# Optimization experiments

Hardware: AMD Instinct MI355X
Metric: run time of the kernel (lower is better)

## Reference

```python
import jax, jax.numpy as jnp
import numpy as np

N = 50000        # nodes
E = 600000       # edges (before self-loops)
IN_DIM = 128
HID = 128
EMB = 128
DEC = 64
B = 1024         # drug pairs
NEG_GAT = 0.2    # GATConv leaky-relu slope
NEG_DEC = 0.1    # decoder LeakyReLU slope
EPS = 1e-5       # BatchNorm eps


def setup_inputs() -> dict:
    key = jax.random.key(0)
    ks = jax.random.split(key, 16)
    rn = lambda k, s, sc=0.05: jax.random.normal(k, s, dtype=jnp.float32) * sc
    return dict(
        x=rn(ks[0], (N, IN_DIM), 1.0),
        edge_index=jax.random.randint(ks[1], (2, E), 0, N, dtype=jnp.int32),
        drug_index=jax.random.randint(ks[2], (B, 2), 1, N + 1, dtype=jnp.int32),
        W1=rn(ks[3], (HID, IN_DIM)), att1=rn(ks[4], (1, 1, 2 * HID)), b1=jnp.zeros((HID,), jnp.float32),
        g1=jnp.ones((HID,), jnp.float32), be1=jnp.zeros((HID,), jnp.float32),
        W2=rn(ks[5], (HID, HID)), att2=rn(ks[6], (1, 1, 2 * HID)), b2=jnp.zeros((HID,), jnp.float32),
        g2=jnp.ones((HID,), jnp.float32), be2=jnp.zeros((HID,), jnp.float32),
        W3=rn(ks[7], (EMB, HID)), att3=rn(ks[8], (1, 1, 2 * EMB)), b3=jnp.zeros((EMB,), jnp.float32),
        g3=jnp.ones((EMB,), jnp.float32), be3=jnp.zeros((EMB,), jnp.float32),
        P1=rn(ks[9], (EMB, DEC), 0.1), P2=rn(ks[10], (DEC, DEC), 0.1),
    )


def _segment_softmax(alpha, seg, n):
    amax = jax.ops.segment_max(alpha, seg, num_segments=n)
    amax = jnp.where(jnp.isfinite(amax), amax, 0.0)
    ex = jnp.exp(alpha - amax[seg])
    den = jax.ops.segment_sum(ex, seg, num_segments=n)
    return ex / (den[seg] + 1e-16)


def _gat(x, src, dst, W, att, b):
    # num_head == 1 (required by original att-parameter shape)
    n = x.shape[0]
    d = W.shape[0]
    h = (x @ W.T)[:, None, :]                    # [N,1,d]
    x_i, x_j = h[dst], h[src]                    # target, source per edge
    # alpha = (cat([x_i,x_j],-1)*att).sum(-1) without materializing the concat
    alpha = (x_i * att[..., :d]).sum(-1) + (x_j * att[..., d:]).sum(-1)  # [E,1]
    alpha = jax.nn.leaky_relu(alpha, NEG_GAT)
    # NOTE: original code softmaxes over edge_index[0] (src) while aggregating by dst
    alpha = _segment_softmax(alpha, src, n)
    out = jax.ops.segment_sum(x_j * alpha[:, :, None], dst, num_segments=n)
    return jax.nn.relu(out.reshape(n, -1) + b)


def _bn(x, g, b):
    # BatchNorm1d (training-mode batch statistics, biased var)
    mu = x.mean(0)
    var = x.var(0)
    return (x - mu) * jax.lax.rsqrt(var + EPS) * g + b


def reference(x, edge_index, drug_index, W1, att1, b1, g1, be1,
              W2, att2, b2, g2, be2, W3, att3, b3, g3, be3, P1, P2):
    n = x.shape[0]
    loops = jnp.arange(n, dtype=edge_index.dtype)
    src = jnp.concatenate([edge_index[0], loops])  # add_self_loops
    dst = jnp.concatenate([edge_index[1], loops])
    h = jax.nn.leaky_relu(_bn(_gat(x, src, dst, W1, att1, b1), g1, be1), NEG_DEC)
    h = jax.nn.leaky_relu(_bn(_gat(h, src, dst, W2, att2, b2), g2, be2), NEG_DEC)
    h = jax.nn.leaky_relu(_bn(_gat(h, src, dst, W3, att3, b3), g3, be3), NEG_DEC)
    a = h[drug_index[:, 0] - 1]                    # [B,EMB]
    bvec = h[drug_index[:, 1] - 1]                 # [B,EMB]
    M = P1 @ P2 @ P1.T                             # [EMB,EMB] bilinear form
    ypred = jnp.einsum('bd,de,be->b', a, M, bvec)[:, None]  # [B,1]
    return ypred
```

## Files before the change

### kernel.cpp

```cpp
#include <hip/hip_runtime.h>
#include <hip/hip_bf16.h>

#define DEVINL __device__ __forceinline__

constexpr int N  = 50000;
constexpr int E  = 600000;
constexpr int TE = E + N;
constexpr int D  = 128;
constexpr int SCAN_B = (N + 255) / 256;
constexpr int GEMM_ROWS = 64;
constexpr int GEMM_B = (N + GEMM_ROWS - 1) / GEMM_ROWS;
constexpr int HST_STRIDE = 136;

typedef short bf16x8 __attribute__((ext_vector_type(8)));
typedef float f32x4  __attribute__((ext_vector_type(4)));

DEVINL float lrelu(float x, float s) { return x >= 0.f ? x : s * x; }

DEVINL unsigned short f2bf(float f) {
    unsigned u = __float_as_uint(f);
    u += 0x7FFFu + ((u >> 16) & 1u);
    return (unsigned short)(u >> 16);
}
DEVINL float bfl(unsigned u) { return __uint_as_float(u << 16); }
DEVINL float bfh(unsigned u) { return __uint_as_float(u & 0xFFFF0000u); }

__global__ __launch_bounds__(256) void k_wb3(const float* __restrict__ W0,
                                             const float* __restrict__ W1,
                                             const float* __restrict__ W2,
                                             unsigned short* __restrict__ Wb) {
    int b = blockIdx.x;
    int l = b >> 6;
    const float* W = (l == 0) ? W0 : (l == 1) ? W1 : W2;
    int t = (b & 63) * 256 + threadIdx.x;
    Wb[l * 16384 + t] = f2bf(W[t]);
}

__global__ __launch_bounds__(256) void k_gemm(const float* __restrict__ X,
                                              const unsigned short* __restrict__ O16,
                                              const unsigned short* __restrict__ Wb,
                                              unsigned short* __restrict__ Hb16,
                                              const float* __restrict__ att,
                                              float* __restrict__ ai,
                                              float* __restrict__ ajx,
                                              const float* __restrict__ csum,
                                              const float* __restrict__ csq,
                                              const float* __restrict__ g,
                                              const float* __restrict__ be,
                                              int apply_bn) {
    __shared__ unsigned short hst[4][16][HST_STRIDE];
    __shared__ float ssl[256];
    int wave = threadIdx.x >> 6, lane = threadIdx.x & 63;
    int m = lane & 15, quad = lane >> 4;
    int r0 = blockIdx.x * GEMM_ROWS + wave * 16;

    if (apply_bn) {
        if (threadIdx.x < 128) {
            int c = threadIdx.x;
            float mean = csum[c] / (float)N;
            float var  = csq[c] / (float)N - mean * mean;
            float scale = g[c] * rsqrtf(var + 1e-5f);
            ssl[c] = scale;
            ssl[128 + c] = be[c] - mean * scale;
        }
        __syncthreads();
    }

    bf16x8 afrag[4];
    int rowA = r0 + m;
    bool rowok = rowA < N;
    #pragma unroll
    for (int k4 = 0; k4 < 4; k4++) {
        int c0 = k4 * 32 + quad * 8;
        float v[8];
        if (rowok) {
            if (apply_bn) {
                uint4 hu = *(const uint4*)(O16 + (size_t)rowA * D + c0);
                v[0] = bfl(hu.x); v[1] = bfh(hu.x);
                v[2] = bfl(hu.y); v[3] = bfh(hu.y);
                v[4] = bfl(hu.z); v[5] = bfh(hu.z);
                v[6] = bfl(hu.w); v[7] = bfh(hu.w);
                #pragma unroll
                for (int j = 0; j < 8; j++)
                    v[j] = lrelu(v[j] * ssl[c0 + j] + ssl[128 + c0 + j], 0.1f);
            } else {
                float4 x0 = *(const float4*)(X + (size_t)rowA * D + c0);
                float4 x1 = *(const float4*)(X + (size_t)rowA * D + c0 + 4);
                v[0] = x0.x; v[1] = x0.y; v[2] = x0.z; v[3] = x0.w;
                v[4] = x1.x; v[5] = x1.y; v[6] = x1.z; v[7] = x1.w;
            }
        } else {
            #pragma unroll
            for (int j = 0; j < 8; j++) v[j] = 0.f;
        }
        #pragma unroll
        for (int j = 0; j < 8; j++) afrag[k4][j] = (short)f2bf(v[j]);
    }

    float pii[4] = {0.f, 0.f, 0.f, 0.f};
    float pjj[4] = {0.f, 0.f, 0.f, 0.f};
    #pragma unroll
    for (int nt = 0; nt < 8; nt++) {
        int n0 = nt * 16;
        f32x4 acc = {0.f, 0.f, 0.f, 0.f};
        const unsigned short* wrow = Wb + (size_t)(n0 + m) * D + quad * 8;
        #pragma unroll
        for (int k4 = 0; k4 < 4; k4++) {
            bf16x8 b = *(const bf16x8*)(wrow + k4 * 32);
            acc = __builtin_amdgcn_mfma_f32_16x16x32_bf16(afrag[k4], b, acc, 0, 0, 0);
        }
        float ad = att[n0 + m];
        float as = att[128 + n0 + m];
        #pragma unroll
        for (int i = 0; i < 4; i++) {
            hst[wave][quad * 4 + i][n0 + m] = f2bf(acc[i]);
            pii[i] += acc[i] * ad;
            pjj[i] += acc[i] * as;
        }
    }

    #pragma unroll
    for (int t = 0; t < 4; t++) {
        int r = t * 4 + quad;
        int row = r0 + r;
        int cb = m * 8;
        uint4 vv = *(const uint4*)&hst[wave][r][cb];
        if (row < N)
            *(uint4*)(Hb16 + (size_t)row * D + cb) = vv;
    }

    #pragma unroll
    for (int mask = 8; mask >= 1; mask >>= 1) {
        #pragma unroll
        for (int i = 0; i < 4; i++) {
            pii[i] += __shfl_xor(pii[i], mask);
            pjj[i] += __shfl_xor(pjj[i], mask);
        }
    }
    if (m == 0) {
        #pragma unroll
        for (int i = 0; i < 4; i++) {
            int row = r0 + quad * 4 + i;
            if (row < N) { ai[row] = pii[i]; ajx[2 * (size_t)row] = pjj[i]; }
        }
    }
}

DEVINL void edge_sd(int e, const int* ei, int& s, int& d) {
    if (e < E) { s = ei[e]; d = ei[E + e]; }
    else       { s = d = e - E; }
}

__global__ __launch_bounds__(256) void k_deg2(const int* __restrict__ ei,
                                              int* __restrict__ degd,
                                              int* __restrict__ degs,
                                              unsigned* __restrict__ rpack) {
    int e = blockIdx.x * 256 + threadIdx.x;
    if (e >= TE) return;
    int s, d; edge_sd(e, ei, s, d);
    int rd = atomicAdd(degd + d, 1);
    int rs = atomicAdd(degs + s, 1);
    rpack[e] = (unsigned)(rd & 0xFFFF) | ((unsigned)rs << 16);
}

__global__ __launch_bounds__(256) void k_scan1(const int* __restrict__ degbase, int* __restrict__ bsum) {
    __shared__ int red[256];
    int arr = blockIdx.x >= SCAN_B;
    int b   = blockIdx.x - arr * SCAN_B;
    const int* deg = degbase + (size_t)arr * N;
    int t = threadIdx.x;
    int v = b * 256 + t;
    red[t] = (v < N) ? deg[v] : 0;
    __syncthreads();
    #pragma unroll
    for (int off = 128; off; off >>= 1) {
        if (t < off) red[t] += red[t + off];
        __syncthreads();
    }
    if (t == 0) bsum[arr * 256 + b] = red[0];
}

__global__ __launch_bounds__(256) void k_scan2(const int* __restrict__ bsum,
                                               int* __restrict__ boff, int* __restrict__ ptrbase) {
    __shared__ int sc[256];
    int t = threadIdx.x;
    for (int arr = 0; arr < 2; arr++) {
        int v = (t < SCAN_B) ? bsum[arr * 256 + t] : 0;
        sc[t] = v;
        __syncthreads();
        #pragma unroll
        for (int off = 1; off < 256; off <<= 1) {
            int add = (t >= off) ? sc[t - off] : 0;
            __syncthreads();
            sc[t] += add;
            __syncthreads();
        }
        if (t < SCAN_B) boff[arr * 256 + t] = sc[t] - v;
        if (t == SCAN_B - 1) ptrbase[(size_t)arr * (N + 8) + N] = sc[t];
        __syncthreads();
    }
}

__global__ __launch_bounds__(256) void k_scan3(const int* __restrict__ degbase,
                                               const int* __restrict__ boff,
                                               int* __restrict__ ptrbase) {
    __shared__ int sc[256];
    int arr = blockIdx.x >= SCAN_B;
    int b   = blockIdx.x - arr * SCAN_B;
    const int* deg = degbase + (size_t)arr * N;
    int* ptr       = ptrbase + (size_t)arr * (N + 8);
    int t = threadIdx.x;
    int v = b * 256 + t;
    int d = (v < N) ? deg[v] : 0;
    sc[t] = d;
    __syncthreads();
    #pragma unroll
    for (int off = 1; off < 256; off <<= 1) {
        int add = (t >= off) ? sc[t - off] : 0;
        __syncthreads();
        sc[t] += add;
        __syncthreads();
    }
    if (v < N) ptr[v] = boff[arr * 256 + b] + sc[t] - d;
}

__global__ __launch_bounds__(256) void k_fill2(const int* __restrict__ ei,
                                               const int* __restrict__ rowp,
                                               const int* __restrict__ srcp,
                                               const unsigned* __restrict__ rpack,
                                               unsigned short* __restrict__ srcc,
                                               unsigned short* __restrict__ dstc) {
    int e = blockIdx.x * 256 + threadIdx.x;
    if (e >= TE) return;
    int s, d; edge_sd(e, ei, s, d);
    unsigned rp = rpack[e];
    srcc[rowp[d] + (int)(rp & 0xFFFFu)] = (unsigned short)s;
    dstc[srcp[s] + (int)(rp >> 16)]     = (unsigned short)d;
}

__global__ __launch_bounds__(256) void k_den(const int* __restrict__ srcp,
                                             const unsigned short* __restrict__ dstc,
                                             const float* __restrict__ ai,
                                             float* __restrict__ ajx,
                                             float* __restrict__ csumz) {
    if (blockIdx.x == 0) csumz[threadIdx.x] = 0.f;
    int g = threadIdx.x >> 4, l16 = threadIdx.x & 15;
    int v = blockIdx.x * 16 + g;
    if (v >= N) return;
    int beg = srcp[v], end = srcp[v + 1];
    float ajv = ajx[2 * (size_t)v];
    float acc = 0.f;
    for (int idx = beg + l16; idx < end; idx += 16) {
        int d = dstc[idx];
        acc += expf(lrelu(ai[d] + ajv, 0.2f));
    }
    #pragma unroll
    for (int mask = 8; mask >= 1; mask >>= 1) acc += __shfl_xor(acc, mask);
    if (l16 == 0) ajx[2 * (size_t)v + 1] = 1.0f / (acc + 1e-16f);
}

__global__ __launch_bounds__(256) void k_aggregate(const int* __restrict__ rowp,
                                                   const unsigned short* __restrict__ srcc,
                                                   const float* __restrict__ ai,
                                                   const float2* __restrict__ ajinv,
                                                   const uint2* __restrict__ Hu2,
                                                   const float* __restrict__ bvec,
                                                   unsigned short* __restrict__ O16) {
    int wid = threadIdx.x >> 6, lane = threadIdx.x & 63;
    int h = lane >> 5, l32 = lane & 31;
    int v = blockIdx.x * 4 + wid;
    if (v >= N) return;
    int beg = rowp[v], end = rowp[v + 1];
    float aiv = ai[v];
    float a0 = 0.f, a1 = 0.f, a2 = 0.f, a3 = 0.f;
    int idx = beg;
    for (; idx + 8 <= end; idx += 8) {
        int    s[4];
        float2 aw[4];
        uint2  u[4];
        #pragma unroll
        for (int t = 0; t < 4; t++) s[t] = srcc[idx + 2 * t + h];
        #pragma unroll
        for (int t = 0; t < 4; t++) aw[t] = ajinv[s[t]];
        #pragma unroll
        for (int t = 0; t < 4; t++) u[t] = Hu2[(size_t)s[t] * 32 + l32];
        #pragma unroll
        for (int t = 0; t < 4; t++) {
            float w = expf(lrelu(aiv + aw[t].x, 0.2f)) * aw[t].y;
            a0 += w * bfl(u[t].x);
            a1 += w * bfh(u[t].x);
            a2 += w * bfl(u[t].y);
            a3 += w * bfh(u[t].y);
        }
    }
    for (; idx + 2 <= end; idx += 2) {
        int s = srcc[idx + h];
        float2 aw = ajinv[s];
        float w = expf(lrelu(aiv + aw.x, 0.2f)) * aw.y;
        uint2 u = Hu2[(size_t)s * 32 + l32];
        a0 += w * bfl(u.x);
        a1 += w * bfh(u.x);
        a2 += w * bfl(u.y);
        a3 += w * bfh(u.y);
    }
    if (idx < end) {
        int s = srcc[idx];
        float2 aw = ajinv[s];
        float w = (h == 0) ? expf(lrelu(aiv + aw.x, 0.2f)) * aw.y : 0.f;
        uint2 u = Hu2[(size_t)s * 32 + l32];
        a0 += w * bfl(u.x);
        a1 += w * bfh(u.x);
        a2 += w * bfl(u.y);
        a3 += w * bfh(u.y);
    }
    a0 += __shfl_xor(a0, 32);
    a1 += __shfl_xor(a1, 32);
    a2 += __shfl_xor(a2, 32);
    a3 += __shfl_xor(a3, 32);
    if (h == 0) {
        float4 b = ((const float4*)bvec)[l32];
        float o0 = fmaxf(a0 + b.x, 0.f);
        float o1 = fmaxf(a1 + b.y, 0.f);
        float o2 = fmaxf(a2 + b.z, 0.f);
        float o3 = fmaxf(a3 + b.w, 0.f);
        uint2 st;
        st.x = (unsigned)f2bf(o0) | ((unsigned)f2bf(o1) << 16);
        st.y = (unsigned)f2bf(o2) | ((unsigned)f2bf(o3) << 16);
        *(uint2*)(O16 + (size_t)v * D + l32 * 4) = st;
    }
}

__global__ __launch_bounds__(256) void k_stats(const unsigned short* __restrict__ O16,
                                               float* __restrict__ colsum, float* __restrict__ colsq) {
    int c4 = (threadIdx.x & 31) * 4;
    int rg = threadIdx.x >> 5;
    float s0=0.f,s1=0.f,s2=0.f,s3=0.f,q0=0.f,q1=0.f,q2=0.f,q3=0.f;
    for (int v = blockIdx.x * 8 + rg; v < N; v += gridDim.x * 8) {
        uint2 u = *(const uint2*)(O16 + (size_t)v * D + c4);
        float v0 = bfl(u.x), v1 = bfh(u.x), v2 = bfl(u.y), v3 = bfh(u.y);
        s0 += v0; q0 += v0 * v0;
        s1 += v1; q1 += v1 * v1;
        s2 += v2; q2 += v2 * v2;
        s3 += v3; q3 += v3 * v3;
    }
    __shared__ float ls[8][128], lq[8][128];
    ls[rg][c4+0]=s0; ls[rg][c4+1]=s1; ls[rg][c4+2]=s2; ls[rg][c4+3]=s3;
    lq[rg][c4+0]=q0; lq[rg][c4+1]=q1; lq[rg][c4+2]=q2; lq[rg][c4+3]=q3;
    __syncthreads();
    if (threadIdx.x < 128) {
        int c = threadIdx.x;
        float s = 0.f, q = 0.f;
        #pragma unroll
        for (int r = 0; r < 8; r++) { s += ls[r][c]; q += lq[r][c]; }
        atomicAdd(colsum + c, s);
        atomicAdd(colsq + c, q);
    }
}

__global__ __launch_bounds__(256) void k_T(const float* __restrict__ P1, const float* __restrict__ P2,
                                           float* __restrict__ T) {
    int t = blockIdx.x * 256 + threadIdx.x;
    if (t >= 128 * 64) return;
    int i = t >> 6, d = t & 63;
    float s = 0.f;
    #pragma unroll 8
    for (int k = 0; k < 64; k++) s += P1[i * 64 + k] * P2[k * 64 + d];
    T[t] = s;
}

__global__ __launch_bounds__(256) void k_M(const float* __restrict__ T, const float* __restrict__ P1,
                                           float* __restrict__ M) {
    int t = blockIdx.x * 256 + threadIdx.x;
    if (t >= 128 * 128) return;
    int i = t >> 7, j = t & 127;
    float s = 0.f;
    #pragma unroll 8
    for (int d = 0; d < 64; d++) s += T[i * 64 + d] * P1[j * 64 + d];
    M[t] = s;
}

__global__ __launch_bounds__(128) void k_pred(const unsigned short* __restrict__ O16,
                                              const float* __restrict__ csum,
                                              const float* __restrict__ csq,
                                              const float* __restrict__ g,
                                              const float* __restrict__ be,
                                              const int* __restrict__ drug,
                                              const float* __restrict__ M,
                                              float* __restrict__ out) {
    int b = blockIdx.x, i = threadIdx.x;
    __shared__ float av[128], bv[128];
    int ia = drug[b * 2] - 1, ib = drug[b * 2 + 1] - 1;
    float mean = csum[i] / (float)N;
    float var  = csq[i] / (float)N - mean * mean;
    float scale = g[i] * rsqrtf(var + 1e-5f);
    float shift = be[i] - mean * scale;
    float ha = __uint_as_float(((unsigned)O16[(size_t)ia * D + i]) << 16);
    float hb = __uint_as_float(((unsigned)O16[(size_t)ib * D + i]) << 16);
    av[i] = lrelu(ha * scale + shift, 0.1f);
    bv[i] = lrelu(hb * scale + shift, 0.1f);
    __syncthreads();
    const float4* M4  = (const float4*)(M + (size_t)i * 128);
    const float4* bv4 = (const float4*)bv;
    float u = 0.f;
    #pragma unroll 8
    for (int j = 0; j < 32; j++) {
        float4 mv = M4[j];
        float4 bb = bv4[j];
        u += mv.x * bb.x + mv.y * bb.y + mv.z * bb.z + mv.w * bb.w;
    }
    float val = av[i] * u;
    #pragma unroll
    for (int off = 32; off; off >>= 1) val += __shfl_down(val, off);
    __shared__ float red[2];
    if ((i & 63) == 0) red[i >> 6] = val;
    __syncthreads();
    if (i == 0) out[b] = red[0] + red[1];
}

extern "C" void kernel_launch(void* const* d_in, const int* in_sizes, int n_in,
                              void* d_out, int out_size, void* d_ws, size_t ws_size,
                              hipStream_t stream) {
    const float* x    = (const float*)d_in[0];
    const int*   ei   = (const int*)  d_in[1];
    const int*   drug = (const int*)  d_in[2];
    const float* W[3]   = {(const float*)d_in[3], (const float*)d_in[8],  (const float*)d_in[13]};
    const float* att[3] = {(const float*)d_in[4], (const float*)d_in[9],  (const float*)d_in[14]};
    const float* bb[3]  = {(const float*)d_in[5], (const float*)d_in[10], (const float*)d_in[15]};
    const float* gg[3]  = {(const float*)d_in[6], (const float*)d_in[11], (const float*)d_in[16]};
    const float* be[3]  = {(const float*)d_in[7], (const float*)d_in[12], (const float*)d_in[17]};
    const float* P1 = (const float*)d_in[18];
    const float* P2 = (const float*)d_in[19];

    float* ws = (float*)d_ws;
    size_t o_H      = 0;
    size_t o_O      = o_H + (size_t)N * 64;
    size_t o_ai     = o_O + (size_t)N * 64;
    size_t o_ajinv  = o_ai + N;
    size_t o_colsum = o_ajinv + 2 * (size_t)N;
    size_t o_colsq  = o_colsum + 128;
    size_t o_deg    = o_colsq + 128;
    size_t o_rpack  = o_deg + 2 * (size_t)N;
    size_t o_rowptr = o_rpack + TE;
    size_t o_srcp   = o_rowptr + N + 8;
    size_t o_src    = o_srcp + N + 8;
    size_t o_dstc   = o_src + TE / 2 + 8;
    size_t o_bsum   = o_dstc + TE / 2 + 8;
    size_t o_boff   = o_bsum + 512;
    size_t o_T      = o_boff + 512;
    size_t o_Mm     = o_T + 128 * 64;
    size_t o_Wb     = o_Mm + 128 * 128;

    unsigned short* Hb16 = (unsigned short*)(ws + o_H);
    uint2*          Hu2  = (uint2*)(ws + o_H);
    unsigned short* O16  = (unsigned short*)(ws + o_O);
    float*    ai    = ws + o_ai;
    float*    ajx   = ws + o_ajinv;
    float2*   ajinv = (float2*)(ws + o_ajinv);
    float*    csum  = ws + o_colsum;
    float*    csq   = ws + o_colsq;
    int*      degd  = (int*)(ws + o_deg);
    int*      degs  = degd + N;
    unsigned* rpack = (unsigned*)(ws + o_rpack);
    int*      rowp  = (int*)(ws + o_rowptr);
    int*      srcp  = (int*)(ws + o_srcp);
    unsigned short* srcc = (unsigned short*)(ws + o_src);
    unsigned short* dstc = (unsigned short*)(ws + o_dstc);
    int*      bsum  = (int*)(ws + o_bsum);
    int*      boff  = (int*)(ws + o_boff);
    float*    Tm    = ws + o_T;
    float*    Mm    = ws + o_Mm;
    unsigned short* Wb = (unsigned short*)(ws + o_Wb);

    const int EB = (TE + 255) / 256;
    const int NB4  = (N + 3) / 4;
    const int NB16 = (N + 15) / 16;

    hipMemsetAsync(degd, 0, (size_t)2 * N * 4, stream);
    k_deg2<<<EB, 256, 0, stream>>>(ei, degd, degs, rpack);
    k_scan1<<<2 * SCAN_B, 256, 0, stream>>>(degd, bsum);
    k_scan2<<<1, 256, 0, stream>>>(bsum, boff, rowp);
    k_scan3<<<2 * SCAN_B, 256, 0, stream>>>(degd, boff, rowp);
    k_fill2<<<EB, 256, 0, stream>>>(ei, rowp, srcp, rpack, srcc, dstc);

    k_wb3<<<192, 256, 0, stream>>>(W[0], W[1], W[2], Wb);

    for (int l = 0; l < 3; l++) {
        k_gemm<<<GEMM_B, 256, 0, stream>>>(x, O16, Wb + l * 16384, Hb16, att[l],
                                           ai, ajx, csum, csq, gg[l == 0 ? 0 : l - 1],
                                           be[l == 0 ? 0 : l - 1], l > 0 ? 1 : 0);
        k_den<<<NB16, 256, 0, stream>>>(srcp, dstc, ai, ajx, csum);
        k_aggregate<<<NB4, 256, 0, stream>>>(rowp, srcc, ai, ajinv, Hu2, bb[l], O16);
        k_stats<<<256, 256, 0, stream>>>(O16, csum, csq);
    }

    k_T<<<32, 256, 0, stream>>>(P1, P2, Tm);
    k_M<<<64, 256, 0, stream>>>(Tm, P1, Mm);
    k_pred<<<1024, 128, 0, stream>>>(O16, csum, csq, gg[2], be[2], drug, Mm, (float*)d_out);
}
```

Measured before the change: 434.1 us.

## Partition degree-count atomics per XCD with workgroup-scope atomics

```diff
diff --git a/kernel.cpp b/kernel.cpp
--- a/kernel.cpp
+++ b/kernel.cpp
@@ -7,6 +7,7 @@
 constexpr int E  = 600000;
 constexpr int TE = E + N;
 constexpr int D  = 128;
+constexpr int NXCD = 8;
 constexpr int SCAN_B = (N + 255) / 256;
 constexpr int GEMM_ROWS = 64;
 constexpr int GEMM_B = (N + GEMM_ROWS - 1) / GEMM_ROWS;
@@ -152,25 +153,41 @@
 }
 
 __global__ __launch_bounds__(256) void k_deg2(const int* __restrict__ ei,
-                                              int* __restrict__ degd,
-                                              int* __restrict__ degs,
+                                              int* __restrict__ part,
                                               unsigned* __restrict__ rpack) {
     int e = blockIdx.x * 256 + threadIdx.x;
     if (e >= TE) return;
+    unsigned xcd;
+    asm volatile("s_getreg_b32 %0, hwreg(HW_REG_XCC_ID)" : "=s"(xcd));
+    xcd &= (NXCD - 1);
     int s, d; edge_sd(e, ei, s, d);
-    int rd = atomicAdd(degd + d, 1);
-    int rs = atomicAdd(degs + s, 1);
-    rpack[e] = (unsigned)(rd & 0xFFFF) | ((unsigned)rs << 16);
-}
-
-__global__ __launch_bounds__(256) void k_scan1(const int* __restrict__ degbase, int* __restrict__ bsum) {
+    int rd = __hip_atomic_fetch_add(part + ((size_t)xcd * N + d), 1,
+                                    __ATOMIC_RELAXED, __HIP_MEMORY_SCOPE_WORKGROUP);
+    int rs = __hip_atomic_fetch_add(part + (((size_t)NXCD + xcd) * N + s), 1,
+                                    __ATOMIC_RELAXED, __HIP_MEMORY_SCOPE_WORKGROUP);
+    rpack[e] = (unsigned)rd | ((unsigned)rs << 13) | (xcd << 26);
+}
+
+__global__ __launch_bounds__(256) void k_scan1(const int* __restrict__ part,
+                                               int* __restrict__ deg,
+                                               unsigned short* __restrict__ cumx,
+                                               int* __restrict__ bsum) {
     __shared__ int red[256];
     int arr = blockIdx.x >= SCAN_B;
     int b   = blockIdx.x - arr * SCAN_B;
-    const int* deg = degbase + (size_t)arr * N;
     int t = threadIdx.x;
     int v = b * 256 + t;
-    red[t] = (v < N) ? deg[v] : 0;
+    int run = 0;
+    if (v < N) {
+        #pragma unroll
+        for (int x = 0; x < NXCD; x++) {
+            size_t o = ((size_t)arr * NXCD + x) * N + v;
+            cumx[o] = (unsigned short)run;
+            run += part[o];
+        }
+        deg[(size_t)arr * N + v] = run;
+    }
+    red[t] = run;
     __syncthreads();
     #pragma unroll
     for (int off = 128; off; off >>= 1) {
@@ -228,14 +245,20 @@
                                                const int* __restrict__ rowp,
                                                const int* __restrict__ srcp,
                                                const unsigned* __restrict__ rpack,
+                                               const unsigned short* __restrict__ cumx,
                                                unsigned short* __restrict__ srcc,
                                                unsigned short* __restrict__ dstc) {
     int e = blockIdx.x * 256 + threadIdx.x;
     if (e >= TE) return;
     int s, d; edge_sd(e, ei, s, d);
     unsigned rp = rpack[e];
-    srcc[rowp[d] + (int)(rp & 0xFFFFu)] = (unsigned short)s;
-    dstc[srcp[s] + (int)(rp >> 16)]     = (unsigned short)d;
+    int rd  = (int)(rp & 0x1FFFu);
+    int rs  = (int)((rp >> 13) & 0x1FFFu);
+    int xcd = (int)(rp >> 26);
+    int posd = rowp[d] + (int)cumx[(size_t)xcd * N + d] + rd;
+    int poss = srcp[s] + (int)cumx[((size_t)NXCD + xcd) * N + s] + rs;
+    srcc[posd] = (unsigned short)s;
+    dstc[poss] = (unsigned short)d;
 }
 
 __global__ __launch_bounds__(256) void k_den(const int* __restrict__ srcp,
@@ -438,8 +461,10 @@
     size_t o_ajinv  = o_ai + N;
     size_t o_colsum = o_ajinv + 2 * (size_t)N;
     size_t o_colsq  = o_colsum + 128;
-    size_t o_deg    = o_colsq + 128;
-    size_t o_rpack  = o_deg + 2 * (size_t)N;
+    size_t o_part   = o_colsq + 128;
+    size_t o_deg    = o_part + 2 * NXCD * (size_t)N;
+    size_t o_cumx   = o_deg + 2 * (size_t)N;
+    size_t o_rpack  = o_cumx + NXCD * (size_t)N;
     size_t o_rowptr = o_rpack + TE;
     size_t o_srcp   = o_rowptr + N + 8;
     size_t o_src    = o_srcp + N + 8;
@@ -458,8 +483,9 @@
     float2*   ajinv = (float2*)(ws + o_ajinv);
     float*    csum  = ws + o_colsum;
     float*    csq   = ws + o_colsq;
-    int*      degd  = (int*)(ws + o_deg);
-    int*      degs  = degd + N;
+    int*      part  = (int*)(ws + o_part);
+    int*      deg   = (int*)(ws + o_deg);
+    unsigned short* cumx = (unsigned short*)(ws + o_cumx);
     unsigned* rpack = (unsigned*)(ws + o_rpack);
     int*      rowp  = (int*)(ws + o_rowptr);
     int*      srcp  = (int*)(ws + o_srcp);
@@ -475,12 +501,12 @@
     const int NB4  = (N + 3) / 4;
     const int NB16 = (N + 15) / 16;
 
-    hipMemsetAsync(degd, 0, (size_t)2 * N * 4, stream);
-    k_deg2<<<EB, 256, 0, stream>>>(ei, degd, degs, rpack);
-    k_scan1<<<2 * SCAN_B, 256, 0, stream>>>(degd, bsum);
+    hipMemsetAsync(part, 0, (size_t)2 * NXCD * N * 4, stream);
+    k_deg2<<<EB, 256, 0, stream>>>(ei, part, rpack);
+    k_scan1<<<2 * SCAN_B, 256, 0, stream>>>(part, deg, cumx, bsum);
     k_scan2<<<1, 256, 0, stream>>>(bsum, boff, rowp);
-    k_scan3<<<2 * SCAN_B, 256, 0, stream>>>(degd, boff, rowp);
-    k_fill2<<<EB, 256, 0, stream>>>(ei, rowp, srcp, rpack, srcc, dstc);
+    k_scan3<<<2 * SCAN_B, 256, 0, stream>>>(deg, boff, rowp);
+    k_fill2<<<EB, 256, 0, stream>>>(ei, rowp, srcp, rpack, cumx, srcc, dstc);
 
     k_wb3<<<192, 256, 0, stream>>>(W[0], W[1], W[2], Wb);
 
```

New measurement: 432.4 us. No clear change (-0.4%).

## Build CSR via two-level bucket sort with shared-memory atomics

Applied to the files above, without the earlier changes.

```diff
diff --git a/kernel.cpp b/kernel.cpp
--- a/kernel.cpp
+++ b/kernel.cpp
@@ -7,10 +7,15 @@
 constexpr int E  = 600000;
 constexpr int TE = E + N;
 constexpr int D  = 128;
-constexpr int SCAN_B = (N + 255) / 256;
 constexpr int GEMM_ROWS = 64;
 constexpr int GEMM_B = (N + GEMM_ROWS - 1) / GEMM_ROWS;
 constexpr int HST_STRIDE = 136;
+
+constexpr int NBUCK = (N + 255) >> 8;
+constexpr int NSB   = 2 * NBUCK;
+constexpr int CHUNK = 2560;
+constexpr int EB3   = (TE + CHUNK - 1) / CHUNK;
+constexpr int EB3P  = 256;
 
 typedef short bf16x8 __attribute__((ext_vector_type(8)));
 typedef float f32x4  __attribute__((ext_vector_type(4)));
@@ -151,91 +156,133 @@
     else       { s = d = e - E; }
 }
 
-__global__ __launch_bounds__(256) void k_deg2(const int* __restrict__ ei,
-                                              int* __restrict__ degd,
-                                              int* __restrict__ degs,
-                                              unsigned* __restrict__ rpack) {
-    int e = blockIdx.x * 256 + threadIdx.x;
-    if (e >= TE) return;
-    int s, d; edge_sd(e, ei, s, d);
-    int rd = atomicAdd(degd + d, 1);
-    int rs = atomicAdd(degs + s, 1);
-    rpack[e] = (unsigned)(rd & 0xFFFF) | ((unsigned)rs << 16);
-}
-
-__global__ __launch_bounds__(256) void k_scan1(const int* __restrict__ degbase, int* __restrict__ bsum) {
-    __shared__ int red[256];
-    int arr = blockIdx.x >= SCAN_B;
-    int b   = blockIdx.x - arr * SCAN_B;
-    const int* deg = degbase + (size_t)arr * N;
+__global__ __launch_bounds__(256) void k_cnt(const int* __restrict__ ei,
+                                             unsigned* __restrict__ hist) {
+    __shared__ unsigned cnt[NSB];
+    for (int t = threadIdx.x; t < NSB; t += 256) cnt[t] = 0;
+    __syncthreads();
+    int base = blockIdx.x * CHUNK;
+    for (int i = threadIdx.x; i < CHUNK; i += 256) {
+        int e = base + i;
+        if (e < TE) {
+            int s, d; edge_sd(e, ei, s, d);
+            atomicAdd(&cnt[d >> 8], 1u);
+            atomicAdd(&cnt[NBUCK + (s >> 8)], 1u);
+        }
+    }
+    __syncthreads();
+    unsigned* row = hist + (size_t)blockIdx.x * NSB;
+    for (int t = threadIdx.x; t < NSB; t += 256) row[t] = cnt[t];
+}
+
+__global__ __launch_bounds__(256) void k_bscan(const unsigned* __restrict__ hist,
+                                               unsigned* __restrict__ pref,
+                                               unsigned* __restrict__ btot) {
+    __shared__ unsigned sc[256];
+    int sb = blockIdx.x, t = threadIdx.x;
+    unsigned v = (t < EB3) ? hist[(size_t)t * NSB + sb] : 0;
+    sc[t] = v;
+    __syncthreads();
+    #pragma unroll
+    for (int off = 1; off < 256; off <<= 1) {
+        unsigned add = (t >= off) ? sc[t - off] : 0;
+        __syncthreads();
+        sc[t] += add;
+        __syncthreads();
+    }
+    if (t < EB3) pref[(size_t)sb * EB3P + t] = sc[t] - v;
+    if (t == EB3 - 1) btot[sb] = sc[t];
+}
+
+__global__ __launch_bounds__(256) void k_boff(const unsigned* __restrict__ btot,
+                                              unsigned* __restrict__ boff2,
+                                              int* __restrict__ ptrbase) {
+    __shared__ unsigned sc[256];
     int t = threadIdx.x;
-    int v = b * 256 + t;
-    red[t] = (v < N) ? deg[v] : 0;
-    __syncthreads();
-    #pragma unroll
-    for (int off = 128; off; off >>= 1) {
-        if (t < off) red[t] += red[t + off];
-        __syncthreads();
-    }
-    if (t == 0) bsum[arr * 256 + b] = red[0];
-}
-
-__global__ __launch_bounds__(256) void k_scan2(const int* __restrict__ bsum,
-                                               int* __restrict__ boff, int* __restrict__ ptrbase) {
-    __shared__ int sc[256];
-    int t = threadIdx.x;
-    for (int arr = 0; arr < 2; arr++) {
-        int v = (t < SCAN_B) ? bsum[arr * 256 + t] : 0;
+    for (int side = 0; side < 2; side++) {
+        unsigned v = (t < NBUCK) ? btot[side * NBUCK + t] : 0;
         sc[t] = v;
         __syncthreads();
         #pragma unroll
         for (int off = 1; off < 256; off <<= 1) {
-            int add = (t >= off) ? sc[t - off] : 0;
+            unsigned add = (t >= off) ? sc[t - off] : 0;
             __syncthreads();
             sc[t] += add;
             __syncthreads();
         }
-        if (t < SCAN_B) boff[arr * 256 + t] = sc[t] - v;
-        if (t == SCAN_B - 1) ptrbase[(size_t)arr * (N + 8) + N] = sc[t];
-        __syncthreads();
-    }
-}
-
-__global__ __launch_bounds__(256) void k_scan3(const int* __restrict__ degbase,
-                                               const int* __restrict__ boff,
-                                               int* __restrict__ ptrbase) {
-    __shared__ int sc[256];
-    int arr = blockIdx.x >= SCAN_B;
-    int b   = blockIdx.x - arr * SCAN_B;
-    const int* deg = degbase + (size_t)arr * N;
-    int* ptr       = ptrbase + (size_t)arr * (N + 8);
-    int t = threadIdx.x;
-    int v = b * 256 + t;
-    int d = (v < N) ? deg[v] : 0;
-    sc[t] = d;
+        if (t < NBUCK) boff2[side * (NBUCK + 1) + t] = sc[t] - v;
+        if (t == NBUCK - 1) boff2[side * (NBUCK + 1) + NBUCK] = sc[t];
+        __syncthreads();
+    }
+    if (t == 0) { ptrbase[N] = TE; ptrbase[(N + 8) + N] = TE; }
+}
+
+__global__ __launch_bounds__(256) void k_scatter(const int* __restrict__ ei,
+                                                 const unsigned* __restrict__ pref,
+                                                 const unsigned* __restrict__ boff2,
+                                                 unsigned* __restrict__ sorted) {
+    __shared__ unsigned alloc[NSB];
+    int j = blockIdx.x;
+    for (int t = threadIdx.x; t < NSB; t += 256) {
+        int side = t >= NBUCK;
+        int bucket = t - side * NBUCK;
+        alloc[t] = boff2[side * (NBUCK + 1) + bucket] + pref[(size_t)t * EB3P + j]
+                 + (side ? (unsigned)TE : 0u);
+    }
+    __syncthreads();
+    int base = j * CHUNK;
+    for (int i = threadIdx.x; i < CHUNK; i += 256) {
+        int e = base + i;
+        if (e < TE) {
+            int s, d; edge_sd(e, ei, s, d);
+            unsigned pd = atomicAdd(&alloc[d >> 8], 1u);
+            sorted[pd] = ((unsigned)(d & 255) << 16) | (unsigned)s;
+            unsigned ps = atomicAdd(&alloc[NBUCK + (s >> 8)], 1u);
+            sorted[ps] = ((unsigned)(s & 255) << 16) | (unsigned)d;
+        }
+    }
+}
+
+__global__ __launch_bounds__(256) void k_csr(const unsigned* __restrict__ sorted,
+                                             const unsigned* __restrict__ boff2,
+                                             int* __restrict__ ptrbase,
+                                             unsigned short* __restrict__ srcc,
+                                             unsigned short* __restrict__ dstc) {
+    __shared__ unsigned cnt[256];
+    __shared__ unsigned sc[256];
+    int sb = blockIdx.x, t = threadIdx.x;
+    int side = sb >= NBUCK;
+    int bucket = sb - side * NBUCK;
+    unsigned beg = boff2[side * (NBUCK + 1) + bucket];
+    unsigned end = boff2[side * (NBUCK + 1) + bucket + 1];
+    const unsigned* srt = sorted + (side ? (size_t)TE : 0);
+    unsigned short* out = side ? dstc : srcc;
+    int* ptr = ptrbase + (size_t)side * (N + 8);
+    cnt[t] = 0;
+    __syncthreads();
+    for (unsigned idx = beg + t; idx < end; idx += 256)
+        atomicAdd(&cnt[srt[idx] >> 16], 1u);
+    __syncthreads();
+    unsigned own = cnt[t];
+    sc[t] = own;
     __syncthreads();
     #pragma unroll
     for (int off = 1; off < 256; off <<= 1) {
-        int add = (t >= off) ? sc[t - off] : 0;
+        unsigned add = (t >= off) ? sc[t - off] : 0;
         __syncthreads();
         sc[t] += add;
         __syncthreads();
     }
-    if (v < N) ptr[v] = boff[arr * 256 + b] + sc[t] - d;
-}
-
-__global__ __launch_bounds__(256) void k_fill2(const int* __restrict__ ei,
-                                               const int* __restrict__ rowp,
-                                               const int* __restrict__ srcp,
-                                               const unsigned* __restrict__ rpack,
-                                               unsigned short* __restrict__ srcc,
-                                               unsigned short* __restrict__ dstc) {
-    int e = blockIdx.x * 256 + threadIdx.x;
-    if (e >= TE) return;
-    int s, d; edge_sd(e, ei, s, d);
-    unsigned rp = rpack[e];
-    srcc[rowp[d] + (int)(rp & 0xFFFFu)] = (unsigned short)s;
-    dstc[srcp[s] + (int)(rp >> 16)]     = (unsigned short)d;
+    unsigned loc = sc[t] - own;
+    int v = (bucket << 8) + t;
+    if (v < N) ptr[v] = (int)(beg + loc);
+    cnt[t] = beg + loc;
+    __syncthreads();
+    for (unsigned idx = beg + t; idx < end; idx += 256) {
+        unsigned u = srt[idx];
+        unsigned pos = atomicAdd(&cnt[u >> 16], 1u);
+        out[pos] = (unsigned short)u;
+    }
 }
 
 __global__ __launch_bounds__(256) void k_den(const int* __restrict__ srcp,
@@ -438,15 +485,16 @@
     size_t o_ajinv  = o_ai + N;
     size_t o_colsum = o_ajinv + 2 * (size_t)N;
     size_t o_colsq  = o_colsum + 128;
-    size_t o_deg    = o_colsq + 128;
-    size_t o_rpack  = o_deg + 2 * (size_t)N;
-    size_t o_rowptr = o_rpack + TE;
+    size_t o_hist   = o_colsq + 128;
+    size_t o_pref   = o_hist + (size_t)EB3 * NSB;
+    size_t o_btot   = o_pref + (size_t)NSB * EB3P;
+    size_t o_boff2  = o_btot + 512;
+    size_t o_sorted = o_boff2 + 512;
+    size_t o_rowptr = o_sorted + 2 * (size_t)TE;
     size_t o_srcp   = o_rowptr + N + 8;
     size_t o_src    = o_srcp + N + 8;
     size_t o_dstc   = o_src + TE / 2 + 8;
-    size_t o_bsum   = o_dstc + TE / 2 + 8;
-    size_t o_boff   = o_bsum + 512;
-    size_t o_T      = o_boff + 512;
+    size_t o_T      = o_dstc + TE / 2 + 8;
     size_t o_Mm     = o_T + 128 * 64;
     size_t o_Wb     = o_Mm + 128 * 128;
 
@@ -458,29 +506,27 @@
     float2*   ajinv = (float2*)(ws + o_ajinv);
     float*    csum  = ws + o_colsum;
     float*    csq   = ws + o_colsq;
-    int*      degd  = (int*)(ws + o_deg);
-    int*      degs  = degd + N;
-    unsigned* rpack = (unsigned*)(ws + o_rpack);
+    unsigned* hist  = (unsigned*)(ws + o_hist);
+    unsigned* pref  = (unsigned*)(ws + o_pref);
+    unsigned* btot  = (unsigned*)(ws + o_btot);
+    unsigned* boff2 = (unsigned*)(ws + o_boff2);
+    unsigned* sorted= (unsigned*)(ws + o_sorted);
     int*      rowp  = (int*)(ws + o_rowptr);
     int*      srcp  = (int*)(ws + o_srcp);
     unsigned short* srcc = (unsigned short*)(ws + o_src);
     unsigned short* dstc = (unsigned short*)(ws + o_dstc);
-    int*      bsum  = (int*)(ws + o_bsum);
-    int*      boff  = (int*)(ws + o_boff);
     float*    Tm    = ws + o_T;
     float*    Mm    = ws + o_Mm;
     unsigned short* Wb = (unsigned short*)(ws + o_Wb);
 
-    const int EB = (TE + 255) / 256;
     const int NB4  = (N + 3) / 4;
     const int NB16 = (N + 15) / 16;
 
-    hipMemsetAsync(degd, 0, (size_t)2 * N * 4, stream);
-    k_deg2<<<EB, 256, 0, stream>>>(ei, degd, degs, rpack);
-    k_scan1<<<2 * SCAN_B, 256, 0, stream>>>(degd, bsum);
-    k_scan2<<<1, 256, 0, stream>>>(bsum, boff, rowp);
-    k_scan3<<<2 * SCAN_B, 256, 0, stream>>>(degd, boff, rowp);
-    k_fill2<<<EB, 256, 0, stream>>>(ei, rowp, srcp, rpack, srcc, dstc);
+    k_cnt    <<<EB3, 256, 0, stream>>>(ei, hist);
+    k_bscan  <<<NSB, 256, 0, stream>>>(hist, pref, btot);
+    k_boff   <<<1,   256, 0, stream>>>(btot, boff2, rowp);
+    k_scatter<<<EB3, 256, 0, stream>>>(ei, pref, boff2, sorted);
+    k_csr    <<<NSB, 256, 0, stream>>>(sorted, boff2, rowp, srcc, dstc);
 
     k_wb3<<<192, 256, 0, stream>>>(W[0], W[1], W[2], Wb);
 
```

Measured after the change: 389.1 us. 10.4% less time.
